# Optimization experiments

Measured on AMD Instinct MI355X. Metric: run time of the kernel, lower is better.

## Reference

```python
import jax, jax.numpy as jnp
import numpy as np

N, E = 10000, 640000
IN_DIM, EDGE_DIM, OUT_DIM = 128, 128, 128


def setup_inputs() -> dict:
    key = jax.random.key(0)
    ks = jax.random.split(key, 9)
    s = 0.02  # init scale for weights
    return {
        "x": jax.random.normal(ks[0], (N, IN_DIM), dtype=jnp.float32),
        "edge_index": jax.random.randint(ks[1], (2, E), 0, N, dtype=jnp.int64),
        "edge_attr": jax.random.normal(ks[2], (E, EDGE_DIM), dtype=jnp.float32),
        "We": jax.random.normal(ks[3], (EDGE_DIM, IN_DIM), dtype=jnp.float32) * s,
        "be": jnp.zeros((IN_DIM,), dtype=jnp.float32),
        "W1": jax.random.normal(ks[4], (2 * IN_DIM, OUT_DIM), dtype=jnp.float32) * s,
        "b1": jnp.zeros((OUT_DIM,), dtype=jnp.float32),
        "W2": jax.random.normal(ks[5], (OUT_DIM, OUT_DIM), dtype=jnp.float32) * s,
        "b2": jnp.zeros((OUT_DIM,), dtype=jnp.float32),
    }


def reference(x, edge_index, edge_attr, We, be, W1, b1, W2, b2):
    src, dst = edge_index[0], edge_index[1]
    num_nodes = x.shape[0]
    # edge_encoder + per-target scatter-add of edge embeddings
    edge_emb = edge_attr @ We + be                                   # [E, in]
    edge_agg = jax.ops.segment_sum(edge_emb, dst, num_segments=num_nodes)  # [N, in]
    x_comb = jnp.concatenate([x, edge_agg], axis=-1)                 # [N, 2*in]
    # GINConv (eps=0): mlp(x_i + sum_{j->i} x_j)
    neigh = jax.ops.segment_sum(x_comb[src], dst, num_segments=num_nodes)  # [N, 2*in]
    h = x_comb + neigh
    return jax.nn.relu(h @ W1 + b1) @ W2 + b2                        # [N, out]
```

## Files before the change

kernel.cpp:

```cpp
#include <hip/hip_runtime.h>
#include <hip/hip_fp16.h>

#define IN_DIM 128
#define TWO_IN 256
#define CAP 192
#define NB 16
#define ONB 16

__global__ void k_prep(const float* __restrict__ We, const float* __restrict__ be,
                       const float* __restrict__ W1, float* __restrict__ W1eff) {
    __shared__ float wes[8][IN_DIM];
    int tid = threadIdx.x;
    int r0 = blockIdx.x * 8;
    for (int i = tid; i < 8 * IN_DIM; i += 128) {
        int m = i >> 7, c = i & 127;
        wes[m][c] = We[(r0 + m) * IN_DIM + c];
    }
    __syncthreads();
    float acc[8];
    #pragma unroll
    for (int m = 0; m < 8; ++m) acc[m] = 0.f;
    for (int c = 0; c < IN_DIM; ++c) {
        float w = W1[(IN_DIM + c) * IN_DIM + tid];
        #pragma unroll
        for (int m = 0; m < 8; ++m) acc[m] += wes[m][c] * w;
    }
    #pragma unroll
    for (int m = 0; m < 8; ++m) {
        W1eff[(IN_DIM + r0 + m) * IN_DIM + tid] = acc[m];
        W1eff[(r0 + m) * IN_DIM + tid] = W1[(r0 + m) * IN_DIM + tid];
    }
    if (blockIdx.x == 0) {
        float va = 0.f;
        for (int c = 0; c < IN_DIM; ++c) va += be[c] * W1[(IN_DIM + c) * IN_DIM + tid];
        W1eff[(size_t)TWO_IN * IN_DIM + tid] = va;
    }
}

__global__ void k_fill(const int* __restrict__ src, const int* __restrict__ dst,
                       int* __restrict__ cnt, int2* __restrict__ slots, int E) {
    int e = blockIdx.x * blockDim.x + threadIdx.x;
    if (e < E) {
        int d = dst[e];
        int pos = atomicAdd(&cnt[d], 1);
        slots[(size_t)d * CAP + pos] = make_int2(src[e], e);
    }
}

__global__ void k_agg(const float* __restrict__ edge_attr,
                      const int2* __restrict__ slots,
                      const int* __restrict__ cnt,
                      float* __restrict__ aggE, int n) {
    int wave = (int)((blockIdx.x * blockDim.x + threadIdx.x) >> 6);
    int lane = threadIdx.x & 63;
    if (wave >= n) return;
    int c = cnt[wave];
    int half = lane >> 5, l = lane & 31;
    const float4* E4 = (const float4*)edge_attr;
    float4 a0 = {0,0,0,0}, a1 = {0,0,0,0}, a2 = {0,0,0,0}, a3 = {0,0,0,0};
    size_t rb = (size_t)wave * CAP;
    for (int b = 0; b < c; b += 64) {
        int rem = min(64, c - b);
        int eid = (b + lane < c) ? slots[rb + b + lane].y : 0;
        int i = 0;
        for (; i + 7 < rem; i += 8) {
            int ea0 = __builtin_amdgcn_readlane(eid, i);
            int eb0 = __builtin_amdgcn_readlane(eid, i + 1);
            int ea1 = __builtin_amdgcn_readlane(eid, i + 2);
            int eb1 = __builtin_amdgcn_readlane(eid, i + 3);
            int ea2 = __builtin_amdgcn_readlane(eid, i + 4);
            int eb2 = __builtin_amdgcn_readlane(eid, i + 5);
            int ea3 = __builtin_amdgcn_readlane(eid, i + 6);
            int eb3 = __builtin_amdgcn_readlane(eid, i + 7);
            int e0 = half ? eb0 : ea0;
            int e1 = half ? eb1 : ea1;
            int e2 = half ? eb2 : ea2;
            int e3 = half ? eb3 : ea3;
            float4 v0 = E4[(size_t)e0 * 32 + l];
            float4 v1 = E4[(size_t)e1 * 32 + l];
            float4 v2 = E4[(size_t)e2 * 32 + l];
            float4 v3 = E4[(size_t)e3 * 32 + l];
            a0.x += v0.x; a0.y += v0.y; a0.z += v0.z; a0.w += v0.w;
            a1.x += v1.x; a1.y += v1.y; a1.z += v1.z; a1.w += v1.w;
            a2.x += v2.x; a2.y += v2.y; a2.z += v2.z; a2.w += v2.w;
            a3.x += v3.x; a3.y += v3.y; a3.z += v3.z; a3.w += v3.w;
        }
        for (; i + 1 < rem; i += 2) {
            int ea = __builtin_amdgcn_readlane(eid, i);
            int eb = __builtin_amdgcn_readlane(eid, i + 1);
            int e0 = half ? eb : ea;
            float4 v0 = E4[(size_t)e0 * 32 + l];
            a0.x += v0.x; a0.y += v0.y; a0.z += v0.z; a0.w += v0.w;
        }
        if (i < rem) {
            int ea = __builtin_amdgcn_readlane(eid, i);
            if (half == 0) {
                float4 v0 = E4[(size_t)ea * 32 + l];
                a0.x += v0.x; a0.y += v0.y; a0.z += v0.z; a0.w += v0.w;
            }
        }
    }
    float4 t;
    t.x = (a0.x + a1.x) + (a2.x + a3.x);
    t.y = (a0.y + a1.y) + (a2.y + a3.y);
    t.z = (a0.z + a1.z) + (a2.z + a3.z);
    t.w = (a0.w + a1.w) + (a2.w + a3.w);
    t.x += __shfl_xor(t.x, 32);
    t.y += __shfl_xor(t.y, 32);
    t.z += __shfl_xor(t.z, 32);
    t.w += __shfl_xor(t.w, 32);
    if (half == 0) ((float4*)aggE)[(size_t)wave * 32 + l] = t;
}

__global__ void k_gemmP(const float* __restrict__ x, const float* __restrict__ aggE,
                        const int* __restrict__ cnt, const float* __restrict__ W1eff,
                        __half* __restrict__ P, int n) {
    __shared__ float hs[NB][TWO_IN];
    __shared__ float degs[NB];
    int tid = threadIdx.x;
    int base = blockIdx.x * NB;
    const float4* X4 = (const float4*)(x + (size_t)base * IN_DIM);
    const float4* A4 = (const float4*)(aggE + (size_t)base * IN_DIM);
    int tot4 = NB * IN_DIM / 4;
    for (int i = tid; i < tot4; i += 128) {
        int m = i >> 5, c = i & 31;
        float4 vx = {0.f,0.f,0.f,0.f}, va = {0.f,0.f,0.f,0.f};
        if (base + m < n) { vx = X4[i]; va = A4[i]; }
        ((float4*)&hs[m][0])[c] = vx;
        ((float4*)&hs[m][IN_DIM])[c] = va;
    }
    if (tid < NB) degs[tid] = (base + tid < n) ? (float)cnt[base + tid] : 0.f;
    __syncthreads();
    float acc[NB];
    #pragma unroll
    for (int m = 0; m < NB; ++m) acc[m] = 0.f;
    for (int k = 0; k < TWO_IN; ++k) {
        float w = W1eff[k * IN_DIM + tid];
        #pragma unroll
        for (int m = 0; m < NB; ++m) acc[m] += hs[m][k] * w;
    }
    float w256 = W1eff[(size_t)TWO_IN * IN_DIM + tid];
    #pragma unroll
    for (int m = 0; m < NB; ++m) {
        int node = base + m;
        if (node < n)
            P[(size_t)node * IN_DIM + tid] = __float2half(acc[m] + degs[m] * w256);
    }
}

__global__ void k_out(const __half* __restrict__ P, const int2* __restrict__ slots,
                      const int* __restrict__ cnt,
                      const float* __restrict__ b1, const float* __restrict__ W2,
                      const float* __restrict__ b2,
                      float* __restrict__ out, int n) {
    __shared__ float hs[ONB][IN_DIM];
    __shared__ float sb1[IN_DIM];
    int tid = threadIdx.x;
    int wid = tid >> 6, lane = tid & 63;
    int half = lane >> 5, l = lane & 31;
    int base = blockIdx.x * ONB;
    if (tid < IN_DIM) sb1[tid] = b1[tid];
    const uint2* P8 = (const uint2*)P;
    #pragma unroll
    for (int j = 0; j < 2; ++j) {
        int m = wid * 2 + j;
        int v = base + m;
        float4 r = {0.f, 0.f, 0.f, 0.f};
        if (v < n) {
            int c = cnt[v];
            size_t rb = (size_t)v * CAP;
            float4 a0 = {0,0,0,0}, a1 = {0,0,0,0}, a2 = {0,0,0,0}, a3 = {0,0,0,0};
            for (int b = 0; b < c; b += 64) {
                int rem = min(64, c - b);
                int sid = (b + lane < c) ? slots[rb + b + lane].x : 0;
                int i = 0;
                for (; i + 7 < rem; i += 8) {
                    int sa0 = __builtin_amdgcn_readlane(sid, i);
                    int sb0 = __builtin_amdgcn_readlane(sid, i + 1);
                    int sa1 = __builtin_amdgcn_readlane(sid, i + 2);
                    int sb1_ = __builtin_amdgcn_readlane(sid, i + 3);
                    int sa2 = __builtin_amdgcn_readlane(sid, i + 4);
                    int sb2 = __builtin_amdgcn_readlane(sid, i + 5);
                    int sa3 = __builtin_amdgcn_readlane(sid, i + 6);
                    int sb3 = __builtin_amdgcn_readlane(sid, i + 7);
                    int s0 = half ? sb0 : sa0;
                    int s1 = half ? sb1_ : sa1;
                    int s2 = half ? sb2 : sa2;
                    int s3 = half ? sb3 : sa3;
                    uint2 u0 = P8[(size_t)s0 * 32 + l];
                    uint2 u1 = P8[(size_t)s1 * 32 + l];
                    uint2 u2 = P8[(size_t)s2 * 32 + l];
                    uint2 u3 = P8[(size_t)s3 * 32 + l];
                    float2 lo, hi;
                    lo = __half22float2(*(const __half2*)&u0.x);
                    hi = __half22float2(*(const __half2*)&u0.y);
                    a0.x += lo.x; a0.y += lo.y; a0.z += hi.x; a0.w += hi.y;
                    lo = __half22float2(*(const __half2*)&u1.x);
                    hi = __half22float2(*(const __half2*)&u1.y);
                    a1.x += lo.x; a1.y += lo.y; a1.z += hi.x; a1.w += hi.y;
                    lo = __half22float2(*(const __half2*)&u2.x);
                    hi = __half22float2(*(const __half2*)&u2.y);
                    a2.x += lo.x; a2.y += lo.y; a2.z += hi.x; a2.w += hi.y;
                    lo = __half22float2(*(const __half2*)&u3.x);
                    hi = __half22float2(*(const __half2*)&u3.y);
                    a3.x += lo.x; a3.y += lo.y; a3.z += hi.x; a3.w += hi.y;
                }
                for (; i + 1 < rem; i += 2) {
                    int sa = __builtin_amdgcn_readlane(sid, i);
                    int sb = __builtin_amdgcn_readlane(sid, i + 1);
                    int s0 = half ? sb : sa;
                    uint2 u0 = P8[(size_t)s0 * 32 + l];
                    float2 lo = __half22float2(*(const __half2*)&u0.x);
                    float2 hi = __half22float2(*(const __half2*)&u0.y);
                    a0.x += lo.x; a0.y += lo.y; a0.z += hi.x; a0.w += hi.y;
                }
                if (i < rem) {
                    int sa = __builtin_amdgcn_readlane(sid, i);
                    if (half == 0) {
                        uint2 u0 = P8[(size_t)sa * 32 + l];
                        float2 lo = __half22float2(*(const __half2*)&u0.x);
                        float2 hi = __half22float2(*(const __half2*)&u0.y);
                        a0.x += lo.x; a0.y += lo.y; a0.z += hi.x; a0.w += hi.y;
                    }
                }
            }
            if (half == 0) {
                uint2 u0 = P8[(size_t)v * 32 + l];
                float2 lo = __half22float2(*(const __half2*)&u0.x);
                float2 hi = __half22float2(*(const __half2*)&u0.y);
                a0.x += lo.x; a0.y += lo.y; a0.z += hi.x; a0.w += hi.y;
            }
            r.x = (a0.x + a1.x) + (a2.x + a3.x);
            r.y = (a0.y + a1.y) + (a2.y + a3.y);
            r.z = (a0.z + a1.z) + (a2.z + a3.z);
            r.w = (a0.w + a1.w) + (a2.w + a3.w);
            r.x += __shfl_xor(r.x, 32);
            r.y += __shfl_xor(r.y, 32);
            r.z += __shfl_xor(r.z, 32);
            r.w += __shfl_xor(r.w, 32);
        }
        if (half == 0 && v < n) ((float4*)&hs[m][0])[l] = r;
    }
    __syncthreads();
    int col = tid & 127, grp = tid >> 7;
    float acc[4] = {0.f, 0.f, 0.f, 0.f};
    for (int k = 0; k < IN_DIM; ++k) {
        float w = W2[k * IN_DIM + col];
        float bb = sb1[k];
        #pragma unroll
        for (int j = 0; j < 4; ++j) {
            float t = hs[grp + 4 * j][k] + bb;
            acc[j] += (t > 0.f ? t : 0.f) * w;
        }
    }
    float b2v = b2[col];
    #pragma unroll
    for (int j = 0; j < 4; ++j) {
        int v = base + grp + 4 * j;
        if (v < n) out[(size_t)v * IN_DIM + col] = acc[j] + b2v;
    }
}

extern "C" void kernel_launch(void* const* d_in, const int* in_sizes, int n_in,
                              void* d_out, int out_size, void* d_ws, size_t ws_size,
                              hipStream_t stream) {
    const float* x         = (const float*)d_in[0];
    const int*   ei        = (const int*)d_in[1];
    const float* edge_attr = (const float*)d_in[2];
    const float* We        = (const float*)d_in[3];
    const float* be        = (const float*)d_in[4];
    const float* W1        = (const float*)d_in[5];
    const float* b1        = (const float*)d_in[6];
    const float* W2        = (const float*)d_in[7];
    const float* b2        = (const float*)d_in[8];
    float* out = (float*)d_out;

    int N = in_sizes[0] / IN_DIM;
    int E = in_sizes[1] / 2;
    const int* src = ei;
    const int* dst = ei + E;

    char* ws = (char*)d_ws;
    size_t o = 0;
    auto take = [&](size_t nbytes) -> void* {
        void* p = (void*)(ws + o);
        o += (nbytes + 255) & ~(size_t)255;
        return p;
    };
    int*    cnt   = (int*)take((size_t)N * 4);
    int2*   slots = (int2*)take(((size_t)N * CAP + 64) * 8);
    float*  aggE  = (float*)take((size_t)N * IN_DIM * 4);
    __half* P     = (__half*)take((size_t)N * IN_DIM * 2);
    float*  W1eff = (float*)take((size_t)(TWO_IN + 1) * IN_DIM * 4);
    (void)ws_size; (void)n_in; (void)out_size;

    int gE = (E + 255) / 256;
    int gW = (N * 64 + 255) / 256;
    int gP = (N + NB - 1) / NB;
    int gO = (N + ONB - 1) / ONB;

    hipMemsetAsync(cnt, 0, (size_t)N * 4, stream);
    k_prep<<<16, 128, 0, stream>>>(We, be, W1, W1eff);
    k_fill<<<gE, 256, 0, stream>>>(src, dst, cnt, slots, E);
    k_agg<<<gW, 256, 0, stream>>>(edge_attr, slots, cnt, aggE, N);
    k_gemmP<<<gP, 128, 0, stream>>>(x, aggE, cnt, W1eff, P, N);
    k_out<<<gO, 512, 0, stream>>>(P, slots, cnt, b1, W2, b2, out, N);
}
```

Baseline: 207.5 us.

## Fuse edge aggregation with first-layer GEMM and fold count reset into prep

Merges the edge-attribute gather-sum kernel and the W1eff projection kernel into one kernel: each 256-thread block aggregates four nodes into shared memory and then computes their projected P rows. This drops the aggE intermediate buffer (write and reread) and one launch. The memset of the count array is moved into the prep kernel, removing another launch. In exchange the GEMM now reuses each W1eff load across only 2 nodes instead of 16, so weight traffic from cache rises.

```diff
diff --git a/kernel.cpp b/kernel.cpp
--- a/kernel.cpp
+++ b/kernel.cpp
@@ -4,14 +4,15 @@
 #define IN_DIM 128
 #define TWO_IN 256
 #define CAP 192
-#define NB 16
 #define ONB 16
 
 __global__ void k_prep(const float* __restrict__ We, const float* __restrict__ be,
-                       const float* __restrict__ W1, float* __restrict__ W1eff) {
+                       const float* __restrict__ W1, float* __restrict__ W1eff,
+                       int* __restrict__ cnt, int n) {
     __shared__ float wes[8][IN_DIM];
     int tid = threadIdx.x;
     int r0 = blockIdx.x * 8;
+    for (int i = blockIdx.x * 128 + tid; i < n; i += 16 * 128) cnt[i] = 0;
     for (int i = tid; i < 8 * IN_DIM; i += 128) {
         int m = i >> 7, c = i & 127;
         wes[m][c] = We[(r0 + m) * IN_DIM + c];
@@ -47,119 +48,105 @@
     }
 }
 
-__global__ void k_agg(const float* __restrict__ edge_attr,
-                      const int2* __restrict__ slots,
-                      const int* __restrict__ cnt,
-                      float* __restrict__ aggE, int n) {
-    int wave = (int)((blockIdx.x * blockDim.x + threadIdx.x) >> 6);
-    int lane = threadIdx.x & 63;
-    if (wave >= n) return;
-    int c = cnt[wave];
+__global__ void __launch_bounds__(256)
+k_aggP(const float* __restrict__ x, const float* __restrict__ edge_attr,
+       const int2* __restrict__ slots, const int* __restrict__ cnt,
+       const float* __restrict__ W1eff, __half* __restrict__ P, int n) {
+    __shared__ float hs[4][TWO_IN];
+    __shared__ float degs[4];
+    int tid = threadIdx.x;
+    int wid = tid >> 6, lane = tid & 63;
     int half = lane >> 5, l = lane & 31;
-    const float4* E4 = (const float4*)edge_attr;
-    float4 a0 = {0,0,0,0}, a1 = {0,0,0,0}, a2 = {0,0,0,0}, a3 = {0,0,0,0};
-    size_t rb = (size_t)wave * CAP;
-    for (int b = 0; b < c; b += 64) {
-        int rem = min(64, c - b);
-        int eid = (b + lane < c) ? slots[rb + b + lane].y : 0;
-        int i = 0;
-        for (; i + 7 < rem; i += 8) {
-            int ea0 = __builtin_amdgcn_readlane(eid, i);
-            int eb0 = __builtin_amdgcn_readlane(eid, i + 1);
-            int ea1 = __builtin_amdgcn_readlane(eid, i + 2);
-            int eb1 = __builtin_amdgcn_readlane(eid, i + 3);
-            int ea2 = __builtin_amdgcn_readlane(eid, i + 4);
-            int eb2 = __builtin_amdgcn_readlane(eid, i + 5);
-            int ea3 = __builtin_amdgcn_readlane(eid, i + 6);
-            int eb3 = __builtin_amdgcn_readlane(eid, i + 7);
-            int e0 = half ? eb0 : ea0;
-            int e1 = half ? eb1 : ea1;
-            int e2 = half ? eb2 : ea2;
-            int e3 = half ? eb3 : ea3;
-            float4 v0 = E4[(size_t)e0 * 32 + l];
-            float4 v1 = E4[(size_t)e1 * 32 + l];
-            float4 v2 = E4[(size_t)e2 * 32 + l];
-            float4 v3 = E4[(size_t)e3 * 32 + l];
-            a0.x += v0.x; a0.y += v0.y; a0.z += v0.z; a0.w += v0.w;
-            a1.x += v1.x; a1.y += v1.y; a1.z += v1.z; a1.w += v1.w;
-            a2.x += v2.x; a2.y += v2.y; a2.z += v2.z; a2.w += v2.w;
-            a3.x += v3.x; a3.y += v3.y; a3.z += v3.z; a3.w += v3.w;
+    int v = blockIdx.x * 4 + wid;
+    if (v < n) {
+        int c = cnt[v];
+        if (lane == 0) degs[wid] = (float)c;
+        float2 xv = ((const float2*)x)[(size_t)v * 64 + lane];
+        ((float2*)&hs[wid][0])[lane] = xv;
+        const float4* E4 = (const float4*)edge_attr;
+        float4 a0 = {0,0,0,0}, a1 = {0,0,0,0}, a2 = {0,0,0,0}, a3 = {0,0,0,0};
+        size_t rb = (size_t)v * CAP;
+        for (int b = 0; b < c; b += 64) {
+            int rem = min(64, c - b);
+            int eid = (b + lane < c) ? slots[rb + b + lane].y : 0;
+            int i = 0;
+            for (; i + 7 < rem; i += 8) {
+                int t0 = __builtin_amdgcn_readlane(eid, i + 0);
+                int t1 = __builtin_amdgcn_readlane(eid, i + 1);
+                int t2 = __builtin_amdgcn_readlane(eid, i + 2);
+                int t3 = __builtin_amdgcn_readlane(eid, i + 3);
+                int t4 = __builtin_amdgcn_readlane(eid, i + 4);
+                int t5 = __builtin_amdgcn_readlane(eid, i + 5);
+                int t6 = __builtin_amdgcn_readlane(eid, i + 6);
+                int t7 = __builtin_amdgcn_readlane(eid, i + 7);
+                int e0 = half ? t1 : t0;
+                int e1 = half ? t3 : t2;
+                int e2 = half ? t5 : t4;
+                int e3 = half ? t7 : t6;
+                float4 v0 = E4[(size_t)e0 * 32 + l];
+                float4 v1 = E4[(size_t)e1 * 32 + l];
+                float4 v2 = E4[(size_t)e2 * 32 + l];
+                float4 v3 = E4[(size_t)e3 * 32 + l];
+                a0.x += v0.x; a0.y += v0.y; a0.z += v0.z; a0.w += v0.w;
+                a1.x += v1.x; a1.y += v1.y; a1.z += v1.z; a1.w += v1.w;
+                a2.x += v2.x; a2.y += v2.y; a2.z += v2.z; a2.w += v2.w;
+                a3.x += v3.x; a3.y += v3.y; a3.z += v3.z; a3.w += v3.w;
+            }
+            for (; i + 1 < rem; i += 2) {
+                int ta = __builtin_amdgcn_readlane(eid, i);
+                int tb = __builtin_amdgcn_readlane(eid, i + 1);
+                int e0 = half ? tb : ta;
+                float4 v0 = E4[(size_t)e0 * 32 + l];
+                a0.x += v0.x; a0.y += v0.y; a0.z += v0.z; a0.w += v0.w;
+            }
+            if (i < rem) {
+                int ta = __builtin_amdgcn_readlane(eid, i);
+                if (half == 0) {
+                    float4 v0 = E4[(size_t)ta * 32 + l];
+                    a0.x += v0.x; a0.y += v0.y; a0.z += v0.z; a0.w += v0.w;
+                }
+            }
         }
-        for (; i + 1 < rem; i += 2) {
-            int ea = __builtin_amdgcn_readlane(eid, i);
-            int eb = __builtin_amdgcn_readlane(eid, i + 1);
-            int e0 = half ? eb : ea;
-            float4 v0 = E4[(size_t)e0 * 32 + l];
-            a0.x += v0.x; a0.y += v0.y; a0.z += v0.z; a0.w += v0.w;
-        }
-        if (i < rem) {
-            int ea = __builtin_amdgcn_readlane(eid, i);
-            if (half == 0) {
-                float4 v0 = E4[(size_t)ea * 32 + l];
-                a0.x += v0.x; a0.y += v0.y; a0.z += v0.z; a0.w += v0.w;
-            }
-        }
-    }
-    float4 t;
-    t.x = (a0.x + a1.x) + (a2.x + a3.x);
-    t.y = (a0.y + a1.y) + (a2.y + a3.y);
-    t.z = (a0.z + a1.z) + (a2.z + a3.z);
-    t.w = (a0.w + a1.w) + (a2.w + a3.w);
-    t.x += __shfl_xor(t.x, 32);
-    t.y += __shfl_xor(t.y, 32);
-    t.z += __shfl_xor(t.z, 32);
-    t.w += __shfl_xor(t.w, 32);
-    if (half == 0) ((float4*)aggE)[(size_t)wave * 32 + l] = t;
-}
-
-__global__ void k_gemmP(const float* __restrict__ x, const float* __restrict__ aggE,
-                        const int* __restrict__ cnt, const float* __restrict__ W1eff,
-                        __half* __restrict__ P, int n) {
-    __shared__ float hs[NB][TWO_IN];
-    __shared__ float degs[NB];
-    int tid = threadIdx.x;
-    int base = blockIdx.x * NB;
-    const float4* X4 = (const float4*)(x + (size_t)base * IN_DIM);
-    const float4* A4 = (const float4*)(aggE + (size_t)base * IN_DIM);
-    int tot4 = NB * IN_DIM / 4;
-    for (int i = tid; i < tot4; i += 128) {
-        int m = i >> 5, c = i & 31;
-        float4 vx = {0.f,0.f,0.f,0.f}, va = {0.f,0.f,0.f,0.f};
-        if (base + m < n) { vx = X4[i]; va = A4[i]; }
-        ((float4*)&hs[m][0])[c] = vx;
-        ((float4*)&hs[m][IN_DIM])[c] = va;
-    }
-    if (tid < NB) degs[tid] = (base + tid < n) ? (float)cnt[base + tid] : 0.f;
+        float4 t;
+        t.x = (a0.x + a1.x) + (a2.x + a3.x);
+        t.y = (a0.y + a1.y) + (a2.y + a3.y);
+        t.z = (a0.z + a1.z) + (a2.z + a3.z);
+        t.w = (a0.w + a1.w) + (a2.w + a3.w);
+        t.x += __shfl_xor(t.x, 32);
+        t.y += __shfl_xor(t.y, 32);
+        t.z += __shfl_xor(t.z, 32);
+        t.w += __shfl_xor(t.w, 32);
+        if (half == 0) ((float4*)&hs[wid][IN_DIM])[l] = t;
+    }
     __syncthreads();
-    float acc[NB];
-    #pragma unroll
-    for (int m = 0; m < NB; ++m) acc[m] = 0.f;
+    int col = tid & 127, g = tid >> 7;
+    int m0 = 2 * g, m1 = 2 * g + 1;
+    float acc0 = 0.f, acc1 = 0.f;
     for (int k = 0; k < TWO_IN; ++k) {
-        float w = W1eff[k * IN_DIM + tid];
-        #pragma unroll
-        for (int m = 0; m < NB; ++m) acc[m] += hs[m][k] * w;
-    }
-    float w256 = W1eff[(size_t)TWO_IN * IN_DIM + tid];
-    #pragma unroll
-    for (int m = 0; m < NB; ++m) {
-        int node = base + m;
-        if (node < n)
-            P[(size_t)node * IN_DIM + tid] = __float2half(acc[m] + degs[m] * w256);
-    }
-}
-
-__global__ void k_out(const __half* __restrict__ P, const int2* __restrict__ slots,
-                      const int* __restrict__ cnt,
-                      const float* __restrict__ b1, const float* __restrict__ W2,
-                      const float* __restrict__ b2,
-                      float* __restrict__ out, int n) {
+        float w = W1eff[k * IN_DIM + col];
+        acc0 += hs[m0][k] * w;
+        acc1 += hs[m1][k] * w;
+    }
+    float w256 = W1eff[(size_t)TWO_IN * IN_DIM + col];
+    int v0 = blockIdx.x * 4 + m0;
+    int v1 = blockIdx.x * 4 + m1;
+    if (v0 < n) P[(size_t)v0 * IN_DIM + col] = __float2half(acc0 + degs[m0] * w256);
+    if (v1 < n) P[(size_t)v1 * IN_DIM + col] = __float2half(acc1 + degs[m1] * w256);
+}
+
+__global__ void __launch_bounds__(512)
+k_out(const __half* __restrict__ P, const int2* __restrict__ slots,
+      const int* __restrict__ cnt,
+      const float* __restrict__ b1, const float* __restrict__ W2,
+      const float* __restrict__ b2,
+      float* __restrict__ out, int n) {
     __shared__ float hs[ONB][IN_DIM];
-    __shared__ float sb1[IN_DIM];
+    __shared__ float sb1v[IN_DIM];
     int tid = threadIdx.x;
     int wid = tid >> 6, lane = tid & 63;
     int half = lane >> 5, l = lane & 31;
     int base = blockIdx.x * ONB;
-    if (tid < IN_DIM) sb1[tid] = b1[tid];
+    if (tid < IN_DIM) sb1v[tid] = b1[tid];
     const uint2* P8 = (const uint2*)P;
     #pragma unroll
     for (int j = 0; j < 2; ++j) {
@@ -175,18 +162,18 @@
                 int sid = (b + lane < c) ? slots[rb + b + lane].x : 0;
                 int i = 0;
                 for (; i + 7 < rem; i += 8) {
-                    int sa0 = __builtin_amdgcn_readlane(sid, i);
-                    int sb0 = __builtin_amdgcn_readlane(sid, i + 1);
-                    int sa1 = __builtin_amdgcn_readlane(sid, i + 2);
-                    int sb1_ = __builtin_amdgcn_readlane(sid, i + 3);
-                    int sa2 = __builtin_amdgcn_readlane(sid, i + 4);
-                    int sb2 = __builtin_amdgcn_readlane(sid, i + 5);
-                    int sa3 = __builtin_amdgcn_readlane(sid, i + 6);
-                    int sb3 = __builtin_amdgcn_readlane(sid, i + 7);
-                    int s0 = half ? sb0 : sa0;
-                    int s1 = half ? sb1_ : sa1;
-                    int s2 = half ? sb2 : sa2;
-                    int s3 = half ? sb3 : sa3;
+                    int t0 = __builtin_amdgcn_readlane(sid, i + 0);
+                    int t1 = __builtin_amdgcn_readlane(sid, i + 1);
+                    int t2 = __builtin_amdgcn_readlane(sid, i + 2);
+                    int t3 = __builtin_amdgcn_readlane(sid, i + 3);
+                    int t4 = __builtin_amdgcn_readlane(sid, i + 4);
+                    int t5 = __builtin_amdgcn_readlane(sid, i + 5);
+                    int t6 = __builtin_amdgcn_readlane(sid, i + 6);
+                    int t7 = __builtin_amdgcn_readlane(sid, i + 7);
+                    int s0 = half ? t1 : t0;
+                    int s1 = half ? t3 : t2;
+                    int s2 = half ? t5 : t4;
+                    int s3 = half ? t7 : t6;
                     uint2 u0 = P8[(size_t)s0 * 32 + l];
                     uint2 u1 = P8[(size_t)s1 * 32 + l];
                     uint2 u2 = P8[(size_t)s2 * 32 + l];
@@ -206,18 +193,18 @@
                     a3.x += lo.x; a3.y += lo.y; a3.z += hi.x; a3.w += hi.y;
                 }
                 for (; i + 1 < rem; i += 2) {
-                    int sa = __builtin_amdgcn_readlane(sid, i);
-                    int sb = __builtin_amdgcn_readlane(sid, i + 1);
-                    int s0 = half ? sb : sa;
+                    int ta = __builtin_amdgcn_readlane(sid, i);
+                    int tb = __builtin_amdgcn_readlane(sid, i + 1);
+                    int s0 = half ? tb : ta;
                     uint2 u0 = P8[(size_t)s0 * 32 + l];
                     float2 lo = __half22float2(*(const __half2*)&u0.x);
                     float2 hi = __half22float2(*(const __half2*)&u0.y);
                     a0.x += lo.x; a0.y += lo.y; a0.z += hi.x; a0.w += hi.y;
                 }
                 if (i < rem) {
-                    int sa = __builtin_amdgcn_readlane(sid, i);
+                    int ta = __builtin_amdgcn_readlane(sid, i);
                     if (half == 0) {
-                        uint2 u0 = P8[(size_t)sa * 32 + l];
+                        uint2 u0 = P8[(size_t)ta * 32 + l];
                         float2 lo = __half22float2(*(const __half2*)&u0.x);
                         float2 hi = __half22float2(*(const __half2*)&u0.y);
                         a0.x += lo.x; a0.y += lo.y; a0.z += hi.x; a0.w += hi.y;
@@ -246,7 +233,7 @@
     float acc[4] = {0.f, 0.f, 0.f, 0.f};
     for (int k = 0; k < IN_DIM; ++k) {
         float w = W2[k * IN_DIM + col];
-        float bb = sb1[k];
+        float bb = sb1v[k];
         #pragma unroll
         for (int j = 0; j < 4; ++j) {
             float t = hs[grp + 4 * j][k] + bb;
@@ -289,20 +276,16 @@
     };
     int*    cnt   = (int*)take((size_t)N * 4);
     int2*   slots = (int2*)take(((size_t)N * CAP + 64) * 8);
-    float*  aggE  = (float*)take((size_t)N * IN_DIM * 4);
     __half* P     = (__half*)take((size_t)N * IN_DIM * 2);
     float*  W1eff = (float*)take((size_t)(TWO_IN + 1) * IN_DIM * 4);
     (void)ws_size; (void)n_in; (void)out_size;
 
     int gE = (E + 255) / 256;
-    int gW = (N * 64 + 255) / 256;
-    int gP = (N + NB - 1) / NB;
+    int gA = (N + 3) / 4;
     int gO = (N + ONB - 1) / ONB;
 
-    hipMemsetAsync(cnt, 0, (size_t)N * 4, stream);
-    k_prep<<<16, 128, 0, stream>>>(We, be, W1, W1eff);
+    k_prep<<<16, 128, 0, stream>>>(We, be, W1, W1eff, cnt, N);
     k_fill<<<gE, 256, 0, stream>>>(src, dst, cnt, slots, E);
-    k_agg<<<gW, 256, 0, stream>>>(edge_attr, slots, cnt, aggE, N);
-    k_gemmP<<<gP, 128, 0, stream>>>(x, aggE, cnt, W1eff, P, N);
+    k_aggP<<<gA, 256, 0, stream>>>(x, edge_attr, slots, cnt, W1eff, P, N);
     k_out<<<gO, 512, 0, stream>>>(P, slots, cnt, b1, W2, b2, out, N);
 }
```

Measured after the change: 186.9 us (median of 2 runs). 9.9% less time.
